# Kernel optimization log

Measured on AMD Instinct MI355X. Metric: run time of the kernel, lower is better.

## Reference

```python
import jax, jax.numpy as jnp
import numpy as np


def setup_inputs() -> dict:
    key = jax.random.key(0)
    ks = jax.random.split(key, 8)
    B, S, H, I = 2, 1025, 3200, 12800
    T = B * S
    # int8 tensors represented as int32, symmetric range [-128, 126]
    hidden_states = jax.random.randint(ks[0], (B, S, H), 0, 255, dtype=jnp.int32) - 127
    scale_in = (jax.random.uniform(ks[1], (T,)) * 0.02 + 1e-4).astype(jnp.float16)
    w1 = jax.random.randint(ks[2], (I, H), 0, 255, dtype=jnp.int32) - 127
    w1_scale = (jax.random.uniform(ks[3], (I,)) * 0.01 + 1e-4).astype(jnp.float32)
    b1 = (jax.random.normal(ks[4], (I,)) * 0.02).astype(jnp.float16)
    w2 = jax.random.randint(ks[5], (H, I), 0, 255, dtype=jnp.int32) - 127
    w2_scale = (jax.random.uniform(ks[6], (H,)) * 0.01 + 1e-4).astype(jnp.float32)
    b2 = (jax.random.normal(ks[7], (H,)) * 0.02).astype(jnp.float16)
    return {"hidden_states": hidden_states, "scale_in": scale_in,
            "w1": w1, "w1_scale": w1_scale, "b1": b1,
            "w2": w2, "w2_scale": w2_scale, "b2": b2}


def _w8a8_linear(x_int, scale_x, w_int, w_scale, bias):
    # int8 GEMM with int32 accumulation, dequant with per-token * per-channel scales
    acc = jnp.matmul(x_int, w_int.T)  # [T, out] int32
    out = acc.astype(jnp.float32) * scale_x[:, None].astype(jnp.float32) * w_scale[None, :]
    return (out + bias.astype(jnp.float32)).astype(jnp.float16)


def _gelu_and_quant(x_f16):
    # fused GELU + per-token dynamic symmetric int8 quantization
    g = jax.nn.gelu(x_f16.astype(jnp.float32), approximate=False)  # [T, I]
    amax = jnp.max(jnp.abs(g), axis=-1)                              # [T]
    scale_act = (amax / 127.0).astype(jnp.float16)
    s = jnp.maximum(scale_act.astype(jnp.float32), 1e-8)
    q = jnp.clip(jnp.round(g / s[:, None]), -128, 127).astype(jnp.int32)
    return q, scale_act


def reference(hidden_states, scale_in, w1, w1_scale, b1, w2, w2_scale, b2):
    B, S, H = hidden_states.shape
    x = hidden_states.reshape(-1, H)               # [T, H] int
    fc1_out = _w8a8_linear(x, scale_in, w1, w1_scale, b1)      # [T, I] fp16
    act_out, scale_act = _gelu_and_quant(fc1_out)              # int8-as-int32, [T] fp16
    fc2_out = _w8a8_linear(act_out, scale_act, w2, w2_scale, b2)  # [T, H] fp16
    return fc2_out
```

## Files before the change

### kernel.cpp

```cpp
#include <hip/hip_runtime.h>
#include <hip/hip_fp16.h>

typedef int v4i __attribute__((ext_vector_type(4)));

#define AS1C(p) ((const __attribute__((address_space(1))) void*)(p))
#define AS3(p)  ((__attribute__((address_space(3))) void*)(p))

__device__ __forceinline__ void stage_tile(const signed char* __restrict__ g, long long ld,
                                           long long rmax, long long r0, int k0,
                                           char* lds, int tid) {
  const int wave = tid >> 6, lane = tid & 63;
#pragma unroll
  for (int p = 0; p < 2; ++p) {
    const int chunk = wave * 2 + p;
    const int row = chunk * 16 + (lane >> 2);
    const int slot = lane & 3;
    const int gslot = slot ^ ((row >> 1) & 3);
    long long rg = r0 + row;
    if (rg > rmax) rg = rmax;
    const signed char* src = g + rg * ld + (long long)k0 + gslot * 16;
    char* dst = lds + chunk * 1024;
    __builtin_amdgcn_global_load_lds(AS1C(src), AS3(dst), 16, 0, 0);
  }
}

template <int EPI>
__launch_bounds__(256, 2)
__global__ void gemm_i8(const signed char* __restrict__ A, const signed char* __restrict__ Bw,
                        int M, int N, int K,
                        const float* __restrict__ scale_tok, const float* __restrict__ wsc,
                        const float* __restrict__ bias,
                        __half* __restrict__ gout, unsigned int* __restrict__ amax,
                        float* __restrict__ fout) {
  __shared__ __align__(16) char lds[2][2][128 * 64];
  const int tid = threadIdx.x;
  const int lane = tid & 63, wave = tid >> 6;
  const int wrow = (wave >> 1) * 64, wcol = (wave & 1) * 64;
  const long long t0 = (long long)blockIdx.y * 128;
  const long long n0 = (long long)blockIdx.x * 128;

  v4i acc[4][4] = {};

  stage_tile(A, K, (long long)M - 1, t0, 0, lds[0][0], tid);
  stage_tile(Bw, K, (long long)N - 1, n0, 0, lds[0][1], tid);
  __syncthreads();

  const int nk = K >> 6;
  int cur = 0;
  const int srow = lane & 15, sseg = lane >> 4;
  for (int kt = 0; kt < nk; ++kt) {
    if (kt + 1 < nk) {
      stage_tile(A, K, (long long)M - 1, t0, (kt + 1) << 6, lds[cur ^ 1][0], tid);
      stage_tile(Bw, K, (long long)N - 1, n0, (kt + 1) << 6, lds[cur ^ 1][1], tid);
    }
    v4i af[4], bf[4];
#pragma unroll
    for (int mi = 0; mi < 4; ++mi) {
      const int r = wrow + mi * 16 + srow;
      const int sl = sseg ^ ((r >> 1) & 3);
      af[mi] = *(const v4i*)&lds[cur][0][r * 64 + sl * 16];
    }
#pragma unroll
    for (int ni = 0; ni < 4; ++ni) {
      const int r = wcol + ni * 16 + srow;
      const int sl = sseg ^ ((r >> 1) & 3);
      bf[ni] = *(const v4i*)&lds[cur][1][r * 64 + sl * 16];
    }
#pragma unroll
    for (int mi = 0; mi < 4; ++mi)
#pragma unroll
      for (int ni = 0; ni < 4; ++ni)
        acc[mi][ni] = __builtin_amdgcn_mfma_i32_16x16x64_i8(af[mi], bf[ni], acc[mi][ni], 0, 0, 0);
    __syncthreads();
    cur ^= 1;
  }

  if (EPI == 0) {
#pragma unroll
    for (int mi = 0; mi < 4; ++mi) {
#pragma unroll
      for (int j = 0; j < 4; ++j) {
        const long long t = t0 + wrow + mi * 16 + (lane >> 4) * 4 + j;
        const bool valid = (t < M);
        const float st = valid ? scale_tok[t] : 0.f;
        float rowmax = 0.f;
#pragma unroll
        for (int ni = 0; ni < 4; ++ni) {
          const long long c = n0 + wcol + ni * 16 + (lane & 15);
          float v = (float)acc[mi][ni][j] * st * wsc[c] + bias[c];
          v = __half2float(__float2half(v));
          const float gl = 0.5f * v * (1.f + erff(v * 0.70710678118654752f));
          rowmax = fmaxf(rowmax, fabsf(gl));
          if (valid) gout[t * (long long)N + c] = __float2half(gl);
        }
#pragma unroll
        for (int m = 1; m < 16; m <<= 1) rowmax = fmaxf(rowmax, __shfl_xor(rowmax, m));
        if (valid && (lane & 15) == 0) atomicMax(&amax[t], __float_as_uint(rowmax));
      }
    }
  } else {
#pragma unroll
    for (int mi = 0; mi < 4; ++mi) {
#pragma unroll
      for (int j = 0; j < 4; ++j) {
        const long long t = t0 + wrow + mi * 16 + (lane >> 4) * 4 + j;
        if (t < M) {
          const float am = __uint_as_float(amax[t]);
          const float st = __half2float(__float2half(am * (1.f / 127.f)));
#pragma unroll
          for (int ni = 0; ni < 4; ++ni) {
            const long long c = n0 + wcol + ni * 16 + (lane & 15);
            const float v = (float)acc[mi][ni][j] * st * wsc[c] + bias[c];
            fout[t * (long long)N + c] = __half2float(__float2half(v));
          }
        }
      }
    }
  }
}

__global__ void pack_all(const int* __restrict__ a, const int* __restrict__ b,
                         const int* __restrict__ c,
                         signed char* __restrict__ pa, signed char* __restrict__ pb,
                         signed char* __restrict__ pc,
                         unsigned int* __restrict__ amax,
                         long long na, long long nb, long long nc, int T) {
  const long long gid = blockIdx.x * (long long)blockDim.x + threadIdx.x;
  if (gid < T) amax[gid] = 0u;
  const long long n4a = na >> 2, n4b = nb >> 2, n4c = nc >> 2;
  const long long tot = n4a + n4b + n4c;
  const long long stride = (long long)gridDim.x * blockDim.x;
  for (long long u = gid; u < tot; u += stride) {
    const int* src; signed char* dst; long long loc;
    if (u < n4a)            { src = a; dst = pa; loc = u; }
    else if (u < n4a + n4b) { src = b; dst = pb; loc = u - n4a; }
    else                    { src = c; dst = pc; loc = u - n4a - n4b; }
    const int4 v = *(const int4*)(src + (loc << 2));
    const unsigned out = (unsigned)(v.x & 0xff) | ((unsigned)(v.y & 0xff) << 8) |
                         ((unsigned)(v.z & 0xff) << 16) | ((unsigned)(v.w & 0xff) << 24);
    *(unsigned*)(dst + (loc << 2)) = out;
  }
}

__global__ void gelu_quant(const __half* __restrict__ g, const unsigned int* __restrict__ amax,
                           signed char* __restrict__ q, long long total, int I) {
  const long long nchunk = total >> 3;
  const long long stride = (long long)gridDim.x * blockDim.x;
  for (long long c = blockIdx.x * (long long)blockDim.x + threadIdx.x; c < nchunk; c += stride) {
    const long long base = c << 3;
    const int t = (int)(base / I);
    const float am = __uint_as_float(amax[t]);
    const float s = fmaxf(__half2float(__float2half(am * (1.f / 127.f))), 1e-8f);
    const float inv = 1.f / s;
    const int4 raw = *(const int4*)(g + base);
    const __half2* h2 = (const __half2*)&raw;
    union { signed char b[8]; int2 v; } u;
#pragma unroll
    for (int k = 0; k < 4; ++k) {
      const float2 f = __half22float2(h2[k]);
      const float q0 = fminf(fmaxf(rintf(f.x * inv), -128.f), 127.f);
      const float q1 = fminf(fmaxf(rintf(f.y * inv), -128.f), 127.f);
      u.b[k * 2]     = (signed char)(int)q0;
      u.b[k * 2 + 1] = (signed char)(int)q1;
    }
    *(int2*)(q + base) = u.v;
  }
}

extern "C" void kernel_launch(void* const* d_in, const int* in_sizes, int n_in,
                              void* d_out, int out_size, void* d_ws, size_t ws_size,
                              hipStream_t stream) {
  const int* hs = (const int*)d_in[0];
  const float* scale_in = (const float*)d_in[1];
  const int* w1 = (const int*)d_in[2];
  const float* w1s = (const float*)d_in[3];
  const float* b1 = (const float*)d_in[4];
  const int* w2 = (const int*)d_in[5];
  const float* w2s = (const float*)d_in[6];
  const float* b2 = (const float*)d_in[7];

  const int T = in_sizes[1];
  const int I = in_sizes[3];
  const int H = in_sizes[6];

  char* ws = (char*)d_ws;
  unsigned int* amax = (unsigned int*)ws;
  signed char* px  = (signed char*)(ws + 16384);
  signed char* pw1 = px + (size_t)T * H;
  signed char* pw2 = pw1 + (size_t)I * H;
  __half* gbuf = (__half*)(pw2 + (size_t)H * I);
  signed char* qbuf = (signed char*)(gbuf + (size_t)T * I);

  const long long nx = (long long)T * H, nw1 = (long long)I * H, nw2 = (long long)H * I;

  pack_all<<<2048, 256, 0, stream>>>(hs, w1, w2, px, pw1, pw2, amax, nx, nw1, nw2, T);

  dim3 g1(I / 128, (T + 127) / 128);
  gemm_i8<0><<<g1, 256, 0, stream>>>(px, pw1, T, I, H, scale_in, w1s, b1, gbuf, amax, nullptr);

  gelu_quant<<<2048, 256, 0, stream>>>(gbuf, amax, qbuf, (long long)T * I, I);

  dim3 g2(H / 128, (T + 127) / 128);
  gemm_i8<1><<<g2, 256, 0, stream>>>(qbuf, pw2, T, H, I, nullptr, w2s, b2, nullptr, amax, (float*)d_out);
}
```

Baseline: 374.9 us.

## Use 256x256 tiles with 512 threads and triple-buffered LDS pipeline

Replaces the 128x128, 256-thread int8 GEMM with a 256x256 tile and 8 waves per block, each wave computing 128x64 of the tile. Operand loads go through a three-stage LDS ring with explicit vmcnt waits, and the inner loop is split into four MFMA phases separated by barriers, with raised wave priority around the MFMA runs. Per-channel scale and bias are hoisted out of the epilogue loops. The aim is more data reuse per LDS byte and better overlap of global-to-LDS copies with compute. The cost is higher register pressure, 96KB of LDS per block, and partial tiles at the edges: T=2050 wastes most of a 256-row tile, and H=3200 is not a multiple of 256, so column guards were added.

```diff
diff --git a/kernel.cpp b/kernel.cpp
--- a/kernel.cpp
+++ b/kernel.cpp
@@ -6,112 +6,189 @@
 #define AS1C(p) ((const __attribute__((address_space(1))) void*)(p))
 #define AS3(p)  ((__attribute__((address_space(3))) void*)(p))
 
-__device__ __forceinline__ void stage_tile(const signed char* __restrict__ g, long long ld,
-                                           long long rmax, long long r0, int k0,
-                                           char* lds, int tid) {
-  const int wave = tid >> 6, lane = tid & 63;
-#pragma unroll
-  for (int p = 0; p < 2; ++p) {
-    const int chunk = wave * 2 + p;
-    const int row = chunk * 16 + (lane >> 2);
-    const int slot = lane & 3;
-    const int gslot = slot ^ ((row >> 1) & 3);
-    long long rg = r0 + row;
-    if (rg > rmax) rg = rmax;
-    const signed char* src = g + rg * ld + (long long)k0 + gslot * 16;
-    char* dst = lds + chunk * 1024;
-    __builtin_amdgcn_global_load_lds(AS1C(src), AS3(dst), 16, 0, 0);
-  }
-}
+#define BARRIER() do { __builtin_amdgcn_s_barrier(); asm volatile("" ::: "memory"); } while (0)
 
 template <int EPI>
-__launch_bounds__(256, 2)
-__global__ void gemm_i8(const signed char* __restrict__ A, const signed char* __restrict__ Bw,
-                        int M, int N, int K,
-                        const float* __restrict__ scale_tok, const float* __restrict__ wsc,
-                        const float* __restrict__ bias,
-                        __half* __restrict__ gout, unsigned int* __restrict__ amax,
-                        float* __restrict__ fout) {
-  __shared__ __align__(16) char lds[2][2][128 * 64];
+__launch_bounds__(512, 2)
+__global__ void gemm_i8_big(const signed char* __restrict__ A, const signed char* __restrict__ Bw,
+                            int M, int N, int K,
+                            const float* __restrict__ scale_tok, const float* __restrict__ wsc,
+                            const float* __restrict__ bias,
+                            __half* __restrict__ gout, unsigned int* __restrict__ amax,
+                            float* __restrict__ fout) {
+  __shared__ __align__(16) char smem[3][32768];
   const int tid = threadIdx.x;
   const int lane = tid & 63, wave = tid >> 6;
-  const int wrow = (wave >> 1) * 64, wcol = (wave & 1) * 64;
-  const long long t0 = (long long)blockIdx.y * 128;
-  const long long n0 = (long long)blockIdx.x * 128;
-
-  v4i acc[4][4] = {};
-
-  stage_tile(A, K, (long long)M - 1, t0, 0, lds[0][0], tid);
-  stage_tile(Bw, K, (long long)N - 1, n0, 0, lds[0][1], tid);
-  __syncthreads();
-
+  const int wavem = wave >> 2, waven = wave & 3;
+  const long long t0 = (long long)blockIdx.y * 256;
+  const long long n0 = (long long)blockIdx.x * 256;
   const int nk = K >> 6;
+
+  const int gs = (((lane & 3) ^ ((lane >> 3) & 3)) << 4);
+  long long rA0 = t0 + wave * 32 + (lane >> 2);
+  long long rA1 = rA0 + 16;
+  rA0 = rA0 > (long long)M - 1 ? (long long)M - 1 : rA0;
+  rA1 = rA1 > (long long)M - 1 ? (long long)M - 1 : rA1;
+  long long rB0 = n0 + wave * 32 + (lane >> 2);
+  long long rB1 = rB0 + 16;
+  rB0 = rB0 > (long long)N - 1 ? (long long)N - 1 : rB0;
+  rB1 = rB1 > (long long)N - 1 ? (long long)N - 1 : rB1;
+  const signed char* pa0 = A + rA0 * K + gs;
+  const signed char* pa1 = A + rA1 * K + gs;
+  const signed char* pb0 = Bw + rB0 * K + gs;
+  const signed char* pb1 = Bw + rB1 * K + gs;
+  const int dstA = wave * 2048;
+
+#define STAGE_A(kk, bufi) do { \
+    __builtin_amdgcn_global_load_lds(AS1C(pa0 + (kk)), AS3(&smem[bufi][dstA]), 16, 0, 0); \
+    __builtin_amdgcn_global_load_lds(AS1C(pa1 + (kk)), AS3(&smem[bufi][dstA + 1024]), 16, 0, 0); \
+  } while (0)
+#define STAGE_B(kk, bufi) do { \
+    __builtin_amdgcn_global_load_lds(AS1C(pb0 + (kk)), AS3(&smem[bufi][16384 + dstA]), 16, 0, 0); \
+    __builtin_amdgcn_global_load_lds(AS1C(pb1 + (kk)), AS3(&smem[bufi][16384 + dstA + 1024]), 16, 0, 0); \
+  } while (0)
+
+  const int lh = lane & 15;
+  const int slot = (((lane >> 4) ^ ((lh >> 1) & 3)) << 4);
+  const int offA = wavem * 8192 + lh * 64 + slot;
+  const int offB = 16384 + waven * 4096 + lh * 64 + slot;
+
+  v4i acc[8][4] = {};
+  v4i a_[8], b_[4];
+
+  STAGE_A(0, 0); STAGE_B(0, 0);
+  if (nk > 1) {
+    STAGE_A(64, 1); STAGE_B(64, 1);
+    asm volatile("s_waitcnt vmcnt(4)" ::: "memory");
+  } else {
+    asm volatile("s_waitcnt vmcnt(0)" ::: "memory");
+  }
+  BARRIER();
+
   int cur = 0;
-  const int srow = lane & 15, sseg = lane >> 4;
-  for (int kt = 0; kt < nk; ++kt) {
-    if (kt + 1 < nk) {
-      stage_tile(A, K, (long long)M - 1, t0, (kt + 1) << 6, lds[cur ^ 1][0], tid);
-      stage_tile(Bw, K, (long long)N - 1, n0, (kt + 1) << 6, lds[cur ^ 1][1], tid);
-    }
-    v4i af[4], bf[4];
-#pragma unroll
-    for (int mi = 0; mi < 4; ++mi) {
-      const int r = wrow + mi * 16 + srow;
-      const int sl = sseg ^ ((r >> 1) & 3);
-      af[mi] = *(const v4i*)&lds[cur][0][r * 64 + sl * 16];
-    }
-#pragma unroll
-    for (int ni = 0; ni < 4; ++ni) {
-      const int r = wcol + ni * 16 + srow;
-      const int sl = sseg ^ ((r >> 1) & 3);
-      bf[ni] = *(const v4i*)&lds[cur][1][r * 64 + sl * 16];
-    }
-#pragma unroll
-    for (int mi = 0; mi < 4; ++mi)
-#pragma unroll
-      for (int ni = 0; ni < 4; ++ni)
-        acc[mi][ni] = __builtin_amdgcn_mfma_i32_16x16x64_i8(af[mi], bf[ni], acc[mi][ni], 0, 0, 0);
-    __syncthreads();
-    cur ^= 1;
-  }
-
+  for (int t = 0; t < nk; ++t) {
+    const int kk2 = (t + 2) << 6;
+    int idx2 = cur + 2; if (idx2 >= 3) idx2 -= 3;
+    const char* base = smem[cur];
+
+    if (t + 2 < nk) {
+      STAGE_A(kk2, idx2);
+      asm volatile("s_waitcnt vmcnt(6)" ::: "memory");
+    } else if (t + 1 < nk) {
+      asm volatile("s_waitcnt vmcnt(4)" ::: "memory");
+    } else {
+      asm volatile("s_waitcnt vmcnt(0)" ::: "memory");
+    }
+    BARRIER();
+    a_[0] = *(const v4i*)(base + offA);
+    a_[1] = *(const v4i*)(base + offA + 1024);
+    a_[2] = *(const v4i*)(base + offA + 2048);
+    a_[3] = *(const v4i*)(base + offA + 3072);
+    b_[0] = *(const v4i*)(base + offB);
+    b_[1] = *(const v4i*)(base + offB + 1024);
+    __builtin_amdgcn_s_setprio(1);
+    acc[0][0] = __builtin_amdgcn_mfma_i32_16x16x64_i8(a_[0], b_[0], acc[0][0], 0, 0, 0);
+    acc[0][1] = __builtin_amdgcn_mfma_i32_16x16x64_i8(a_[0], b_[1], acc[0][1], 0, 0, 0);
+    acc[1][0] = __builtin_amdgcn_mfma_i32_16x16x64_i8(a_[1], b_[0], acc[1][0], 0, 0, 0);
+    acc[1][1] = __builtin_amdgcn_mfma_i32_16x16x64_i8(a_[1], b_[1], acc[1][1], 0, 0, 0);
+    acc[2][0] = __builtin_amdgcn_mfma_i32_16x16x64_i8(a_[2], b_[0], acc[2][0], 0, 0, 0);
+    acc[2][1] = __builtin_amdgcn_mfma_i32_16x16x64_i8(a_[2], b_[1], acc[2][1], 0, 0, 0);
+    acc[3][0] = __builtin_amdgcn_mfma_i32_16x16x64_i8(a_[3], b_[0], acc[3][0], 0, 0, 0);
+    acc[3][1] = __builtin_amdgcn_mfma_i32_16x16x64_i8(a_[3], b_[1], acc[3][1], 0, 0, 0);
+    __builtin_amdgcn_s_setprio(0);
+    BARRIER();
+
+    if (t + 2 < nk) STAGE_B(kk2, idx2);
+    a_[4] = *(const v4i*)(base + offA + 4096);
+    a_[5] = *(const v4i*)(base + offA + 5120);
+    a_[6] = *(const v4i*)(base + offA + 6144);
+    a_[7] = *(const v4i*)(base + offA + 7168);
+    __builtin_amdgcn_s_setprio(1);
+    acc[4][0] = __builtin_amdgcn_mfma_i32_16x16x64_i8(a_[4], b_[0], acc[4][0], 0, 0, 0);
+    acc[4][1] = __builtin_amdgcn_mfma_i32_16x16x64_i8(a_[4], b_[1], acc[4][1], 0, 0, 0);
+    acc[5][0] = __builtin_amdgcn_mfma_i32_16x16x64_i8(a_[5], b_[0], acc[5][0], 0, 0, 0);
+    acc[5][1] = __builtin_amdgcn_mfma_i32_16x16x64_i8(a_[5], b_[1], acc[5][1], 0, 0, 0);
+    acc[6][0] = __builtin_amdgcn_mfma_i32_16x16x64_i8(a_[6], b_[0], acc[6][0], 0, 0, 0);
+    acc[6][1] = __builtin_amdgcn_mfma_i32_16x16x64_i8(a_[6], b_[1], acc[6][1], 0, 0, 0);
+    acc[7][0] = __builtin_amdgcn_mfma_i32_16x16x64_i8(a_[7], b_[0], acc[7][0], 0, 0, 0);
+    acc[7][1] = __builtin_amdgcn_mfma_i32_16x16x64_i8(a_[7], b_[1], acc[7][1], 0, 0, 0);
+    __builtin_amdgcn_s_setprio(0);
+    BARRIER();
+
+    b_[2] = *(const v4i*)(base + offB + 2048);
+    b_[3] = *(const v4i*)(base + offB + 3072);
+    __builtin_amdgcn_s_setprio(1);
+    acc[0][2] = __builtin_amdgcn_mfma_i32_16x16x64_i8(a_[0], b_[2], acc[0][2], 0, 0, 0);
+    acc[0][3] = __builtin_amdgcn_mfma_i32_16x16x64_i8(a_[0], b_[3], acc[0][3], 0, 0, 0);
+    acc[1][2] = __builtin_amdgcn_mfma_i32_16x16x64_i8(a_[1], b_[2], acc[1][2], 0, 0, 0);
+    acc[1][3] = __builtin_amdgcn_mfma_i32_16x16x64_i8(a_[1], b_[3], acc[1][3], 0, 0, 0);
+    acc[2][2] = __builtin_amdgcn_mfma_i32_16x16x64_i8(a_[2], b_[2], acc[2][2], 0, 0, 0);
+    acc[2][3] = __builtin_amdgcn_mfma_i32_16x16x64_i8(a_[2], b_[3], acc[2][3], 0, 0, 0);
+    acc[3][2] = __builtin_amdgcn_mfma_i32_16x16x64_i8(a_[3], b_[2], acc[3][2], 0, 0, 0);
+    acc[3][3] = __builtin_amdgcn_mfma_i32_16x16x64_i8(a_[3], b_[3], acc[3][3], 0, 0, 0);
+    __builtin_amdgcn_s_setprio(0);
+    BARRIER();
+
+    __builtin_amdgcn_s_setprio(1);
+    acc[4][2] = __builtin_amdgcn_mfma_i32_16x16x64_i8(a_[4], b_[2], acc[4][2], 0, 0, 0);
+    acc[4][3] = __builtin_amdgcn_mfma_i32_16x16x64_i8(a_[4], b_[3], acc[4][3], 0, 0, 0);
+    acc[5][2] = __builtin_amdgcn_mfma_i32_16x16x64_i8(a_[5], b_[2], acc[5][2], 0, 0, 0);
+    acc[5][3] = __builtin_amdgcn_mfma_i32_16x16x64_i8(a_[5], b_[3], acc[5][3], 0, 0, 0);
+    acc[6][2] = __builtin_amdgcn_mfma_i32_16x16x64_i8(a_[6], b_[2], acc[6][2], 0, 0, 0);
+    acc[6][3] = __builtin_amdgcn_mfma_i32_16x16x64_i8(a_[6], b_[3], acc[6][3], 0, 0, 0);
+    acc[7][2] = __builtin_amdgcn_mfma_i32_16x16x64_i8(a_[7], b_[2], acc[7][2], 0, 0, 0);
+    acc[7][3] = __builtin_amdgcn_mfma_i32_16x16x64_i8(a_[7], b_[3], acc[7][3], 0, 0, 0);
+    __builtin_amdgcn_s_setprio(0);
+    BARRIER();
+
+    cur += 1; if (cur >= 3) cur = 0;
+  }
+#undef STAGE_A
+#undef STAGE_B
+
+  long long cidx[4]; float w4[4], bi4[4]; bool cok[4];
+#pragma unroll
+  for (int ni = 0; ni < 4; ++ni) {
+    cidx[ni] = n0 + waven * 64 + ni * 16 + lh;
+    cok[ni] = cidx[ni] < N;
+    w4[ni] = cok[ni] ? wsc[cidx[ni]] : 0.f;
+    bi4[ni] = cok[ni] ? bias[cidx[ni]] : 0.f;
+  }
   if (EPI == 0) {
 #pragma unroll
-    for (int mi = 0; mi < 4; ++mi) {
+    for (int mi = 0; mi < 8; ++mi) {
 #pragma unroll
       for (int j = 0; j < 4; ++j) {
-        const long long t = t0 + wrow + mi * 16 + (lane >> 4) * 4 + j;
-        const bool valid = (t < M);
+        const long long t = t0 + wavem * 128 + mi * 16 + (lane >> 4) * 4 + j;
+        const bool valid = t < M;
         const float st = valid ? scale_tok[t] : 0.f;
         float rowmax = 0.f;
 #pragma unroll
         for (int ni = 0; ni < 4; ++ni) {
-          const long long c = n0 + wcol + ni * 16 + (lane & 15);
-          float v = (float)acc[mi][ni][j] * st * wsc[c] + bias[c];
+          float v = (float)acc[mi][ni][j] * st * w4[ni] + bi4[ni];
           v = __half2float(__float2half(v));
           const float gl = 0.5f * v * (1.f + erff(v * 0.70710678118654752f));
           rowmax = fmaxf(rowmax, fabsf(gl));
-          if (valid) gout[t * (long long)N + c] = __float2half(gl);
+          if (valid && cok[ni]) gout[t * (long long)N + cidx[ni]] = __float2half(gl);
         }
 #pragma unroll
         for (int m = 1; m < 16; m <<= 1) rowmax = fmaxf(rowmax, __shfl_xor(rowmax, m));
-        if (valid && (lane & 15) == 0) atomicMax(&amax[t], __float_as_uint(rowmax));
+        if (valid && lh == 0) atomicMax(&amax[t], __float_as_uint(rowmax));
       }
     }
   } else {
 #pragma unroll
-    for (int mi = 0; mi < 4; ++mi) {
+    for (int mi = 0; mi < 8; ++mi) {
 #pragma unroll
       for (int j = 0; j < 4; ++j) {
-        const long long t = t0 + wrow + mi * 16 + (lane >> 4) * 4 + j;
+        const long long t = t0 + wavem * 128 + mi * 16 + (lane >> 4) * 4 + j;
         if (t < M) {
           const float am = __uint_as_float(amax[t]);
           const float st = __half2float(__float2half(am * (1.f / 127.f)));
 #pragma unroll
           for (int ni = 0; ni < 4; ++ni) {
-            const long long c = n0 + wcol + ni * 16 + (lane & 15);
-            const float v = (float)acc[mi][ni][j] * st * wsc[c] + bias[c];
-            fout[t * (long long)N + c] = __half2float(__float2half(v));
+            const float v = (float)acc[mi][ni][j] * st * w4[ni] + bi4[ni];
+            if (cok[ni]) fout[t * (long long)N + cidx[ni]] = __half2float(__float2half(v));
           }
         }
       }
@@ -195,11 +272,11 @@
 
   pack_all<<<2048, 256, 0, stream>>>(hs, w1, w2, px, pw1, pw2, amax, nx, nw1, nw2, T);
 
-  dim3 g1(I / 128, (T + 127) / 128);
-  gemm_i8<0><<<g1, 256, 0, stream>>>(px, pw1, T, I, H, scale_in, w1s, b1, gbuf, amax, nullptr);
+  dim3 g1(I / 256, (T + 255) / 256);
+  gemm_i8_big<0><<<g1, 512, 0, stream>>>(px, pw1, T, I, H, scale_in, w1s, b1, gbuf, amax, nullptr);
 
   gelu_quant<<<2048, 256, 0, stream>>>(gbuf, amax, qbuf, (long long)T * I, I);
 
-  dim3 g2(H / 128, (T + 127) / 128);
-  gemm_i8<1><<<g2, 256, 0, stream>>>(qbuf, pw2, T, H, I, nullptr, w2s, b2, nullptr, amax, (float*)d_out);
-}
+  dim3 g2((H + 255) / 256, (T + 255) / 256);
+  gemm_i8_big<1><<<g2, 512, 0, stream>>>(qbuf, pw2, T, H, I, nullptr, w2s, b2, nullptr, amax, (float*)d_out);
+}
```

Result: slower. 470.0 us (+25.4%).

## Widen GEMM tiles to 256 columns with triple-buffered LDS and XCD-aware block remap

Applied to the files above, without the earlier changes.

Replaces the int8 GEMM with a version that uses 128x256 (fc1) or 64x256 (fc2) tiles, giving each wave 8 column fragments for more MFMA reuse per LDS load. It uses a 3-stage LDS ring with explicit vmcnt waits so loads run two k-steps ahead, and remaps block IDs round-robin across 8 XCDs with M-major ordering for L2 locality. Scale and bias loads are hoisted out of the epilogue loops. Trade-offs are higher register pressure (MI*8 accumulators) and larger LDS (3 buffers) that may reduce occupancy, and the fc2 grid now needs column bounds checks because H is not a multiple of 256.

```diff
diff --git a/kernel.cpp b/kernel.cpp
--- a/kernel.cpp
+++ b/kernel.cpp
@@ -5,113 +5,153 @@
 
 #define AS1C(p) ((const __attribute__((address_space(1))) void*)(p))
 #define AS3(p)  ((__attribute__((address_space(3))) void*)(p))
-
-__device__ __forceinline__ void stage_tile(const signed char* __restrict__ g, long long ld,
-                                           long long rmax, long long r0, int k0,
-                                           char* lds, int tid) {
-  const int wave = tid >> 6, lane = tid & 63;
-#pragma unroll
-  for (int p = 0; p < 2; ++p) {
-    const int chunk = wave * 2 + p;
-    const int row = chunk * 16 + (lane >> 2);
-    const int slot = lane & 3;
-    const int gslot = slot ^ ((row >> 1) & 3);
-    long long rg = r0 + row;
-    if (rg > rmax) rg = rmax;
-    const signed char* src = g + rg * ld + (long long)k0 + gslot * 16;
-    char* dst = lds + chunk * 1024;
-    __builtin_amdgcn_global_load_lds(AS1C(src), AS3(dst), 16, 0, 0);
-  }
-}
-
-template <int EPI>
+#define BARRIER() do { __builtin_amdgcn_s_barrier(); asm volatile("" ::: "memory"); } while (0)
+
+template <int EPI, int BM>
 __launch_bounds__(256, 2)
-__global__ void gemm_i8(const signed char* __restrict__ A, const signed char* __restrict__ Bw,
+__global__ void gemm_p2(const signed char* __restrict__ A, const signed char* __restrict__ Bw,
                         int M, int N, int K,
                         const float* __restrict__ scale_tok, const float* __restrict__ wsc,
                         const float* __restrict__ bias,
                         __half* __restrict__ gout, unsigned int* __restrict__ amax,
                         float* __restrict__ fout) {
-  __shared__ __align__(16) char lds[2][2][128 * 64];
+  constexpr int ACH = BM / 16;
+  constexpr int CT  = ACH + 16;
+  constexpr int CPW = CT / 4;
+  constexpr int MI  = BM / 32;
+  constexpr int TB  = CT * 1024;
+  __shared__ __align__(16) char smem[3 * TB];
+
   const int tid = threadIdx.x;
   const int lane = tid & 63, wave = tid >> 6;
-  const int wrow = (wave >> 1) * 64, wcol = (wave & 1) * 64;
-  const long long t0 = (long long)blockIdx.y * 128;
-  const long long n0 = (long long)blockIdx.x * 128;
-
-  v4i acc[4][4] = {};
-
-  stage_tile(A, K, (long long)M - 1, t0, 0, lds[0][0], tid);
-  stage_tile(Bw, K, (long long)N - 1, n0, 0, lds[0][1], tid);
-  __syncthreads();
-
+  const int wavem = wave >> 1, waven = wave & 1;
+
+  const int gy = gridDim.y;
+  int lid;
+  {
+    const int o = blockIdx.y * gridDim.x + blockIdx.x;
+    const int nwg = gridDim.x * gy;
+    const int q = nwg >> 3, r = nwg & 7;
+    const int x = o & 7, p = o >> 3;
+    lid = (x < r ? x * (q + 1) : r * (q + 1) + (x - r) * q) + p;
+  }
+  const long long t0 = (long long)(lid % gy) * BM;
+  const long long n0 = (long long)(lid / gy) * 256;
   const int nk = K >> 6;
+
+  const signed char* sp[CPW];
+  int dst[CPW];
+#pragma unroll
+  for (int i = 0; i < CPW; ++i) {
+    const int c = wave * CPW + i;
+    const bool isA = c < ACH;
+    const int lr = (isA ? c : c - ACH) * 16 + (lane >> 2);
+    const int gslot = (((lane & 3) ^ ((lr >> 1) & 3)) << 4);
+    long long gr = isA ? (t0 + lr) : (n0 + lr);
+    const long long rmax = (isA ? (long long)M : (long long)N) - 1;
+    if (gr > rmax) gr = rmax;
+    sp[i] = (isA ? A : Bw) + gr * (long long)K + gslot;
+    dst[i] = c * 1024;
+  }
+
+#define STAGE(bi) do { \
+    _Pragma("unroll") \
+    for (int i = 0; i < CPW; ++i) { \
+      __builtin_amdgcn_global_load_lds(AS1C(sp[i]), AS3(&smem[(bi) * TB + dst[i]]), 16, 0, 0); \
+      sp[i] += 64; \
+    } \
+  } while (0)
+
+  const int lh = lane & 15;
+  const int xs = (((lane >> 4) ^ ((lh >> 1) & 3)) << 4);
+  const int offA = wavem * (BM / 2) * 64 + lh * 64 + xs;
+  const int offB = ACH * 1024 + waven * 8192 + lh * 64 + xs;
+
+  v4i acc[MI][8] = {};
+  v4i a_[MI], b_[8];
+
+  STAGE(0);
+  if (nk > 1) {
+    STAGE(1);
+    if constexpr (CPW == 6) asm volatile("s_waitcnt vmcnt(6)" ::: "memory");
+    else                    asm volatile("s_waitcnt vmcnt(5)" ::: "memory");
+  } else {
+    asm volatile("s_waitcnt vmcnt(0)" ::: "memory");
+  }
+  BARRIER();
+
   int cur = 0;
-  const int srow = lane & 15, sseg = lane >> 4;
-  for (int kt = 0; kt < nk; ++kt) {
-    if (kt + 1 < nk) {
-      stage_tile(A, K, (long long)M - 1, t0, (kt + 1) << 6, lds[cur ^ 1][0], tid);
-      stage_tile(Bw, K, (long long)N - 1, n0, (kt + 1) << 6, lds[cur ^ 1][1], tid);
-    }
-    v4i af[4], bf[4];
-#pragma unroll
-    for (int mi = 0; mi < 4; ++mi) {
-      const int r = wrow + mi * 16 + srow;
-      const int sl = sseg ^ ((r >> 1) & 3);
-      af[mi] = *(const v4i*)&lds[cur][0][r * 64 + sl * 16];
-    }
-#pragma unroll
-    for (int ni = 0; ni < 4; ++ni) {
-      const int r = wcol + ni * 16 + srow;
-      const int sl = sseg ^ ((r >> 1) & 3);
-      bf[ni] = *(const v4i*)&lds[cur][1][r * 64 + sl * 16];
-    }
-#pragma unroll
-    for (int mi = 0; mi < 4; ++mi)
-#pragma unroll
-      for (int ni = 0; ni < 4; ++ni)
-        acc[mi][ni] = __builtin_amdgcn_mfma_i32_16x16x64_i8(af[mi], bf[ni], acc[mi][ni], 0, 0, 0);
-    __syncthreads();
-    cur ^= 1;
-  }
-
+  for (int t = 0; t < nk; ++t) {
+    const char* base = &smem[cur * TB];
+    int b2 = cur + 2; if (b2 >= 3) b2 -= 3;
+    const bool pf = (t + 2) < nk;
+
+    if (pf) STAGE(b2);
+#pragma unroll
+    for (int mi = 0; mi < MI; ++mi) a_[mi] = *(const v4i*)(base + offA + mi * 1024);
+#pragma unroll
+    for (int ni = 0; ni < 8; ++ni) b_[ni] = *(const v4i*)(base + offB + ni * 1024);
+#pragma unroll
+    for (int mi = 0; mi < MI; ++mi)
+#pragma unroll
+      for (int ni = 0; ni < 8; ++ni)
+        acc[mi][ni] = __builtin_amdgcn_mfma_i32_16x16x64_i8(a_[mi], b_[ni], acc[mi][ni], 0, 0, 0);
+
+    asm volatile("s_waitcnt lgkmcnt(0)" ::: "memory");
+    if (pf) {
+      if constexpr (CPW == 6) asm volatile("s_waitcnt vmcnt(6)" ::: "memory");
+      else                    asm volatile("s_waitcnt vmcnt(5)" ::: "memory");
+    } else {
+      asm volatile("s_waitcnt vmcnt(0)" ::: "memory");
+    }
+    BARRIER();
+    cur += 1; if (cur >= 3) cur = 0;
+  }
+#undef STAGE
+
+  long long cidx[8]; float w8[8], bi8[8]; bool cok[8];
+#pragma unroll
+  for (int ni = 0; ni < 8; ++ni) {
+    cidx[ni] = n0 + waven * 128 + ni * 16 + lh;
+    cok[ni] = cidx[ni] < N;
+    w8[ni] = cok[ni] ? wsc[cidx[ni]] : 0.f;
+    bi8[ni] = cok[ni] ? bias[cidx[ni]] : 0.f;
+  }
   if (EPI == 0) {
 #pragma unroll
-    for (int mi = 0; mi < 4; ++mi) {
+    for (int mi = 0; mi < MI; ++mi) {
 #pragma unroll
       for (int j = 0; j < 4; ++j) {
-        const long long t = t0 + wrow + mi * 16 + (lane >> 4) * 4 + j;
-        const bool valid = (t < M);
+        const long long t = t0 + wavem * (BM / 2) + mi * 16 + (lane >> 4) * 4 + j;
+        const bool valid = t < M;
         const float st = valid ? scale_tok[t] : 0.f;
         float rowmax = 0.f;
 #pragma unroll
-        for (int ni = 0; ni < 4; ++ni) {
-          const long long c = n0 + wcol + ni * 16 + (lane & 15);
-          float v = (float)acc[mi][ni][j] * st * wsc[c] + bias[c];
+        for (int ni = 0; ni < 8; ++ni) {
+          float v = (float)acc[mi][ni][j] * st * w8[ni] + bi8[ni];
           v = __half2float(__float2half(v));
           const float gl = 0.5f * v * (1.f + erff(v * 0.70710678118654752f));
           rowmax = fmaxf(rowmax, fabsf(gl));
-          if (valid) gout[t * (long long)N + c] = __float2half(gl);
+          if (valid && cok[ni]) gout[t * (long long)N + cidx[ni]] = __float2half(gl);
         }
 #pragma unroll
         for (int m = 1; m < 16; m <<= 1) rowmax = fmaxf(rowmax, __shfl_xor(rowmax, m));
-        if (valid && (lane & 15) == 0) atomicMax(&amax[t], __float_as_uint(rowmax));
+        if (valid && lh == 0) atomicMax(&amax[t], __float_as_uint(rowmax));
       }
     }
   } else {
 #pragma unroll
-    for (int mi = 0; mi < 4; ++mi) {
+    for (int mi = 0; mi < MI; ++mi) {
 #pragma unroll
       for (int j = 0; j < 4; ++j) {
-        const long long t = t0 + wrow + mi * 16 + (lane >> 4) * 4 + j;
+        const long long t = t0 + wavem * (BM / 2) + mi * 16 + (lane >> 4) * 4 + j;
         if (t < M) {
           const float am = __uint_as_float(amax[t]);
           const float st = __half2float(__float2half(am * (1.f / 127.f)));
 #pragma unroll
-          for (int ni = 0; ni < 4; ++ni) {
-            const long long c = n0 + wcol + ni * 16 + (lane & 15);
-            const float v = (float)acc[mi][ni][j] * st * wsc[c] + bias[c];
-            fout[t * (long long)N + c] = __half2float(__float2half(v));
+          for (int ni = 0; ni < 8; ++ni) {
+            const float v = (float)acc[mi][ni][j] * st * w8[ni] + bi8[ni];
+            if (cok[ni]) fout[t * (long long)N + cidx[ni]] = __half2float(__float2half(v));
           }
         }
       }
@@ -195,11 +235,11 @@
 
   pack_all<<<2048, 256, 0, stream>>>(hs, w1, w2, px, pw1, pw2, amax, nx, nw1, nw2, T);
 
-  dim3 g1(I / 128, (T + 127) / 128);
-  gemm_i8<0><<<g1, 256, 0, stream>>>(px, pw1, T, I, H, scale_in, w1s, b1, gbuf, amax, nullptr);
+  dim3 g1(I / 256, (T + 127) / 128);
+  gemm_p2<0, 128><<<g1, 256, 0, stream>>>(px, pw1, T, I, H, scale_in, w1s, b1, gbuf, amax, nullptr);
 
   gelu_quant<<<2048, 256, 0, stream>>>(gbuf, amax, qbuf, (long long)T * I, I);
 
-  dim3 g2(H / 128, (T + 127) / 128);
-  gemm_i8<1><<<g2, 256, 0, stream>>>(qbuf, pw2, T, H, I, nullptr, w2s, b2, nullptr, amax, (float*)d_out);
-}
+  dim3 g2((H + 255) / 256, (T + 63) / 64);
+  gemm_p2<1, 64><<<g2, 256, 0, stream>>>(qbuf, pw2, T, H, I, nullptr, w2s, b2, nullptr, amax, (float*)d_out);
+}
```

New measurement: 415.2 us. 1.11x slower.
